# Kernel tuning notes

Measured on AMD Instinct MI355X. Metric: run time of the kernel, lower is better.

## Reference

```python
import jax, jax.numpy as jnp
import numpy as np

H = 16  # n_head

def _rotate_half(x):
    d = x.shape[-1] // 2
    return jnp.concatenate([-x[..., d:], x[..., :d]], axis=-1)

def setup_inputs() -> dict:
    key = jax.random.key(0)
    ks = jax.random.split(key, 12)
    b, t, f, h = 8, 1024, 1024, H
    d = f // h
    inp = {
        "query": jax.random.normal(ks[0], (b, t, f), jnp.float32),
        "key": jax.random.normal(ks[1], (b, t, f), jnp.float32),
        "value": jax.random.normal(ks[2], (b, t, f), jnp.float32),
    }
    # realistic rotary cos/sin, shape (t,1,1,d_k)
    inv_freq = 1.0 / (10000.0 ** (np.arange(0, d, 2, dtype=np.float32) / d))
    pos = np.arange(t, dtype=np.float32)[:, None] * inv_freq[None, :]  # (t, d/2)
    emb = np.concatenate([pos, pos], axis=-1)  # (t, d)
    inp["cos"] = jnp.asarray(np.cos(emb)).reshape(t, 1, 1, d)
    inp["sin"] = jnp.asarray(np.sin(emb)).reshape(t, 1, 1, d)
    inp["mask"] = jax.random.randint(ks[3], (b, t, t), 0, 2) > 0
    s = 1.0 / np.sqrt(f)
    inp["Wq"] = jax.random.normal(ks[4], (f, f), jnp.float32) * s
    inp["bq"] = jax.random.normal(ks[5], (f,), jnp.float32) * 0.02
    inp["Wk"] = jax.random.normal(ks[6], (f, f), jnp.float32) * s
    inp["bk"] = jax.random.normal(ks[7], (f,), jnp.float32) * 0.02
    inp["Wv"] = jax.random.normal(ks[8], (f, f), jnp.float32) * s
    inp["bv"] = jax.random.normal(ks[9], (f,), jnp.float32) * 0.02
    inp["Wo"] = jax.random.normal(ks[10], (f, f), jnp.float32) * s
    inp["bo"] = jax.random.normal(ks[11], (f,), jnp.float32) * 0.02
    return inp

def reference(query, key, value, cos, sin, mask, Wq, bq, Wk, bk, Wv, bv, Wo, bo):
    b, t, f = query.shape
    h = H
    d = f // h
    # RoPE applied pre-projection, per-head layout (b,t,h,d)
    c = cos.reshape(1, t, 1, d)  # broadcast over batch and heads
    s = sin.reshape(1, t, 1, d)
    qr = query.reshape(b, t, h, d)
    kr = key.reshape(b, t, h, d)
    qr = qr * c + _rotate_half(qr) * s
    kr = kr * c + _rotate_half(kr) * s
    q_in = qr.reshape(b, t, f)
    k_in = kr.reshape(b, t, f)
    # QKV projections (nn.Linear: x @ W.T + b), then split heads -> (b,h,t,d)
    q = (jnp.einsum('btf,gf->btg', q_in, Wq) + bq).reshape(b, t, h, d).transpose(0, 2, 1, 3)
    k = (jnp.einsum('btf,gf->btg', k_in, Wk) + bk).reshape(b, t, h, d).transpose(0, 2, 1, 3)
    v = (jnp.einsum('btf,gf->btg', value, Wv) + bv).reshape(b, t, h, d).transpose(0, 2, 1, 3)
    scores = jnp.einsum('bhqd,bhkd->bhqk', q, k) / jnp.sqrt(jnp.asarray(d, q.dtype))
    m = mask[:, None, :, :]  # (b,1,t,t)
    scores = jnp.where(m, jnp.asarray(-10000.0, scores.dtype), scores)
    attn = jax.nn.softmax(scores, axis=-1)
    attn = jnp.where(m, jnp.asarray(0.0, attn.dtype), attn)
    out = jnp.einsum('bhqk,bhkd->bhqd', attn, v)  # (b,h,t,d)
    out = out.transpose(0, 2, 1, 3).reshape(b, t, f)
    return jnp.einsum('btf,gf->btg', out, Wo) + bo
```

## Files before the change

### kernel.cpp

```cpp
#include <hip/hip_runtime.h>
#include <stdint.h>

typedef short short8 __attribute__((ext_vector_type(8)));
typedef float f32x4 __attribute__((ext_vector_type(4)));
typedef unsigned short ushort4v __attribute__((ext_vector_type(4)));
typedef unsigned long long u64;

__device__ __forceinline__ unsigned short f2bf(float f) {
  union { float f; unsigned u; } v; v.f = f;
  unsigned r = v.u + 0x7fffu + ((v.u >> 16) & 1u);
  return (unsigned short)(r >> 16);
}

__device__ __forceinline__ void gld_lds16(const void* g, void* l) {
  __builtin_amdgcn_global_load_lds((const __attribute__((address_space(1))) void*)g,
                                   (__attribute__((address_space(3))) void*)l, 16, 0, 0);
}

__global__ void mask_pack(const int* __restrict__ mask, u64* __restrict__ bits) {
  const int tid = blockIdx.x * 256 + threadIdx.x;
  const int w = tid >> 6, lane = tid & 63;
  const int v = mask[(size_t)w * 64 + lane];
  const u64 b = __ballot(v != 0);
  if (lane == 0) bits[w] = b;
}

__global__ void rope_kernel(const float* __restrict__ q, const float* __restrict__ k,
                            const float* __restrict__ cs, const float* __restrict__ sn,
                            unsigned short* __restrict__ qo, unsigned short* __restrict__ ko) {
  const int idx = blockIdx.x * 256 + threadIdx.x;
  const int p   = idx & 7;
  const int bth = idx >> 3;
  const int t   = (bth >> 4) & 1023;
  const size_t base = (size_t)bth * 64;
  const int dd0 = p * 4;

  const float4 x0 = *(const float4*)(q + base + dd0);
  const float4 x1 = *(const float4*)(q + base + dd0 + 32);
  const float4 y0 = *(const float4*)(k + base + dd0);
  const float4 y1 = *(const float4*)(k + base + dd0 + 32);
  const float4 c0 = *(const float4*)(cs + t * 64 + dd0);
  const float4 c1 = *(const float4*)(cs + t * 64 + dd0 + 32);
  const float4 s0 = *(const float4*)(sn + t * 64 + dd0);
  const float4 s1 = *(const float4*)(sn + t * 64 + dd0 + 32);

  ushort4v qlo, qhi, klo, khi;
  qlo[0]=f2bf(x0.x*c0.x - x1.x*s0.x); qlo[1]=f2bf(x0.y*c0.y - x1.y*s0.y);
  qlo[2]=f2bf(x0.z*c0.z - x1.z*s0.z); qlo[3]=f2bf(x0.w*c0.w - x1.w*s0.w);
  qhi[0]=f2bf(x1.x*c1.x + x0.x*s1.x); qhi[1]=f2bf(x1.y*c1.y + x0.y*s1.y);
  qhi[2]=f2bf(x1.z*c1.z + x0.z*s1.z); qhi[3]=f2bf(x1.w*c1.w + x0.w*s1.w);
  klo[0]=f2bf(y0.x*c0.x - y1.x*s0.x); klo[1]=f2bf(y0.y*c0.y - y1.y*s0.y);
  klo[2]=f2bf(y0.z*c0.z - y1.z*s0.z); klo[3]=f2bf(y0.w*c0.w - y1.w*s0.w);
  khi[0]=f2bf(y1.x*c1.x + y0.x*s1.x); khi[1]=f2bf(y1.y*c1.y + y0.y*s1.y);
  khi[2]=f2bf(y1.z*c1.z + y0.z*s1.z); khi[3]=f2bf(y1.w*c1.w + y0.w*s1.w);

  *(ushort4v*)(qo + base + dd0)      = qlo;
  *(ushort4v*)(qo + base + dd0 + 32) = qhi;
  *(ushort4v*)(ko + base + dd0)      = klo;
  *(ushort4v*)(ko + base + dd0 + 32) = khi;
}

__global__ void cast_kernel(const float* __restrict__ src, unsigned short* __restrict__ dst, int n4) {
  const int i = blockIdx.x * 256 + threadIdx.x;
  if (i < n4) {
    const float4 v = *(const float4*)(src + (size_t)i * 4);
    ushort4v o;
    o[0]=f2bf(v.x); o[1]=f2bf(v.y); o[2]=f2bf(v.z); o[3]=f2bf(v.w);
    *(ushort4v*)(dst + (size_t)i * 4) = o;
  }
}

__global__ void cast4_kernel(const float* __restrict__ s0, const float* __restrict__ s1,
                             const float* __restrict__ s2, const float* __restrict__ s3,
                             unsigned short* __restrict__ d0, unsigned short* __restrict__ d1,
                             unsigned short* __restrict__ d2, unsigned short* __restrict__ d3) {
  const int m = blockIdx.y;
  const float* src = (m == 0) ? s0 : (m == 1) ? s1 : (m == 2) ? s2 : s3;
  unsigned short* dst = (m == 0) ? d0 : (m == 1) ? d1 : (m == 2) ? d2 : d3;
  const int i = blockIdx.x * 256 + threadIdx.x;
  const float4 v = *(const float4*)(src + (size_t)i * 4);
  ushort4v o;
  o[0]=f2bf(v.x); o[1]=f2bf(v.y); o[2]=f2bf(v.z); o[3]=f2bf(v.w);
  *(ushort4v*)(dst + (size_t)i * 4) = o;
}

template <int MODE>
__global__ __launch_bounds__(256, 2) void gemm_bt(
    const unsigned short* __restrict__ A, const unsigned short* __restrict__ Bw,
    const float* __restrict__ bias, void* __restrict__ C) {
  constexpr int K = 1024, N = 1024;
  const int tid = threadIdx.x;
  const int wave = tid >> 6, lane = tid & 63;
  const int m0 = blockIdx.x * 128, n0 = blockIdx.y * 128;
  __shared__ unsigned short Asm[128 * 64];
  __shared__ unsigned short Bsm[128 * 64];
  f32x4 acc[4][4] = {};
  const int wr = (wave >> 1) * 64, wc = (wave & 1) * 64;
  const int ld_row = lane >> 3;
  const int ld_col = ((lane & 7) ^ ld_row) * 8;
  const int fr = lane & 15, g = lane >> 4;
  const int fr7 = fr & 7;

  for (int k0 = 0; k0 < K; k0 += 64) {
#pragma unroll
    for (int j = 0; j < 4; ++j) {
      const int c = j * 4 + wave;
      gld_lds16(A  + (size_t)(m0 + 8 * c + ld_row) * K + k0 + ld_col, &Asm[c * 512]);
      gld_lds16(Bw + (size_t)(n0 + 8 * c + ld_row) * K + k0 + ld_col, &Bsm[c * 512]);
    }
    __syncthreads();
#pragma unroll
    for (int ks = 0; ks < 2; ++ks) {
      const int ch = ((ks * 4 + g) ^ fr7) * 8;
      short8 af[4], bf[4];
#pragma unroll
      for (int i = 0; i < 4; ++i)
        af[i] = *(const short8*)&Asm[(wr + i * 16 + fr) * 64 + ch];
#pragma unroll
      for (int i = 0; i < 4; ++i)
        bf[i] = *(const short8*)&Bsm[(wc + i * 16 + fr) * 64 + ch];
#pragma unroll
      for (int i = 0; i < 4; ++i)
#pragma unroll
        for (int j = 0; j < 4; ++j)
          acc[i][j] = __builtin_amdgcn_mfma_f32_16x16x32_bf16(af[i], bf[j], acc[i][j], 0, 0, 0);
    }
    __syncthreads();
  }

#pragma unroll
  for (int i = 0; i < 4; ++i) {
    const int row_base = m0 + wr + i * 16 + g * 4;
#pragma unroll
    for (int j = 0; j < 4; ++j) {
      const int col = n0 + wc + j * 16 + fr;
      const float bval = bias[col];
      if (MODE == 0) {
        float* Co = (float*)C;
#pragma unroll
        for (int r = 0; r < 4; ++r)
          Co[(size_t)(row_base + r) * N + col] = acc[i][j][r] + bval;
      } else if (MODE == 1) {
        unsigned short* Co = (unsigned short*)C;
        const int h_i = col >> 6, dd = col & 63;
#pragma unroll
        for (int r = 0; r < 4; ++r) {
          const int row = row_base + r;
          const int b_i = row >> 10, t_i = row & 1023;
          Co[((size_t)(b_i * 16 + h_i) * 1024 + t_i) * 64 + dd] = f2bf(acc[i][j][r] + bval);
        }
      } else {
        unsigned short* Co = (unsigned short*)C;
        const int h_i = col >> 6, dd = col & 63;
        const int b_i = row_base >> 10, t_i = row_base & 1023;
        ushort4v pk;
        pk[0] = f2bf(acc[i][j][0] + bval); pk[1] = f2bf(acc[i][j][1] + bval);
        pk[2] = f2bf(acc[i][j][2] + bval); pk[3] = f2bf(acc[i][j][3] + bval);
        *(ushort4v*)&Co[((size_t)(b_i * 16 + h_i) * 64 + dd) * 1024 + t_i] = pk;
      }
    }
  }
}

__global__ __launch_bounds__(256, 2) void flash_attn(
    const unsigned short* __restrict__ Qp, const unsigned short* __restrict__ Kp,
    const unsigned short* __restrict__ Vt, const u64* __restrict__ mbits,
    unsigned short* __restrict__ O) {
  const int bh = blockIdx.x & 127, b_i = bh >> 4, h_i = bh & 15;
  const int q0 = (blockIdx.x >> 7) * 128;
  const int tid = threadIdx.x, wave = tid >> 6, lane = tid & 63;
  const unsigned short* Qb = Qp + (size_t)bh * 65536;
  const unsigned short* Kb = Kp + (size_t)bh * 65536;
  const unsigned short* Vb = Vt + (size_t)bh * 65536;
  const u64* mb = mbits + (size_t)b_i * 16384;

  __shared__ unsigned short smem[16640];
  unsigned short* Vsm = smem;
  unsigned short* Ksm = smem + 8192;
  unsigned short* Pw  = smem + 8192 + wave * 2112;

  const int fr = lane & 15, g = lane >> 4, fr7 = fr & 7;
  const int qw = q0 + wave * 32;

  short8 qf[2][2];
#pragma unroll
  for (int mt = 0; mt < 2; ++mt)
#pragma unroll
    for (int ks = 0; ks < 2; ++ks)
      qf[mt][ks] = *(const short8*)&Qb[(size_t)(qw + mt * 16 + fr) * 64 + ks * 32 + g * 8];

  f32x4 o_acc[2][4] = {};
  float l_run[2][4] = {};

  const int kld_row = lane >> 3;
  const int kld_col = ((lane & 7) ^ kld_row) * 8;
  const int vld_row = lane >> 4;
  const int vld_r7w = 4 * (wave & 1) + vld_row;
  const int vld_col = ((lane & 15) ^ vld_r7w) * 8;

  for (int kt = 0; kt < 1024; kt += 128) {
#pragma unroll
    for (int j = 0; j < 4; ++j) {
      const int c = j * 4 + wave;
      gld_lds16(Kb + (size_t)(kt + 8 * c + kld_row) * 64 + kld_col, &Ksm[c * 512]);
      gld_lds16(Vb + (size_t)(4 * c + vld_row) * 1024 + kt + vld_col, &Vsm[c * 512]);
    }
    __syncthreads();

    f32x4 s_acc[2][8] = {};
#pragma unroll
    for (int ks = 0; ks < 2; ++ks) {
      const int ch = ((ks * 4 + g) ^ fr7) * 8;
      short8 kf[8];
#pragma unroll
      for (int nt = 0; nt < 8; ++nt)
        kf[nt] = *(const short8*)&Ksm[(nt * 16 + fr) * 64 + ch];
#pragma unroll
      for (int mt = 0; mt < 2; ++mt)
#pragma unroll
        for (int nt = 0; nt < 8; ++nt)
          s_acc[mt][nt] = __builtin_amdgcn_mfma_f32_16x16x32_bf16(qf[mt][ks], kf[nt], s_acc[mt][nt], 0, 0, 0);
    }
    __syncthreads();

#pragma unroll
    for (int mt = 0; mt < 2; ++mt) {
#pragma unroll
      for (int r = 0; r < 4; ++r) {
        const int qrow = qw + mt * 16 + g * 4 + r;
        const u64* mrow = &mb[(size_t)qrow * 16 + (kt >> 6)];
        const u64 w0 = mrow[0], w1 = mrow[1];
        float lp = l_run[mt][r];
#pragma unroll
        for (int nt = 0; nt < 8; ++nt) {
          const u64 w = (nt < 4) ? w0 : w1;
          float p = exp2f(s_acc[mt][nt][r] * 0.18033688f);
          p = ((w >> ((nt & 3) * 16 + fr)) & 1) ? 0.0f : p;
          lp += p;
          Pw[(g * 4 + r) * 132 + nt * 16 + fr] = f2bf(p);
        }
        l_run[mt][r] = lp;
      }

#pragma unroll
      for (int ks2 = 0; ks2 < 4; ++ks2) {
        const int vch = ((ks2 * 4 + g) ^ fr7) * 8;
        short8 vf[4];
#pragma unroll
        for (int dt = 0; dt < 4; ++dt)
          vf[dt] = *(const short8*)&Vsm[(dt * 16 + fr) * 128 + vch];
        const short8 pf = *(const short8*)&Pw[fr * 132 + ks2 * 32 + g * 8];
#pragma unroll
        for (int dt = 0; dt < 4; ++dt)
          o_acc[mt][dt] = __builtin_amdgcn_mfma_f32_16x16x32_bf16(pf, vf[dt], o_acc[mt][dt], 0, 0, 0);
      }
    }
    __syncthreads();
  }

#pragma unroll
  for (int mt = 0; mt < 2; ++mt)
#pragma unroll
    for (int r = 0; r < 4; ++r) {
      float l = l_run[mt][r];
#pragma unroll
      for (int off = 1; off < 16; off <<= 1) l += __shfl_xor(l, off, 16);
      const float inv_l = 1.0f / l;
      const int qrow = qw + mt * 16 + g * 4 + r;
#pragma unroll
      for (int dt = 0; dt < 4; ++dt) {
        const int dcol = dt * 16 + fr;
        O[((size_t)(b_i * 1024 + qrow)) * 1024 + h_i * 64 + dcol] = f2bf(o_acc[mt][dt][r] * inv_l);
      }
    }
}

extern "C" void kernel_launch(void* const* d_in, const int* in_sizes, int n_in,
                              void* d_out, int out_size, void* d_ws, size_t ws_size,
                              hipStream_t stream) {
  const float* query = (const float*)d_in[0];
  const float* key   = (const float*)d_in[1];
  const float* value = (const float*)d_in[2];
  const float* cosb  = (const float*)d_in[3];
  const float* sinb  = (const float*)d_in[4];
  const int*   mask  = (const int*)d_in[5];
  const float* Wq = (const float*)d_in[6];
  const float* bq = (const float*)d_in[7];
  const float* Wk = (const float*)d_in[8];
  const float* bk = (const float*)d_in[9];
  const float* Wv = (const float*)d_in[10];
  const float* bv = (const float*)d_in[11];
  const float* Wo = (const float*)d_in[12];
  const float* bo = (const float*)d_in[13];
  (void)in_sizes; (void)n_in; (void)out_size; (void)ws_size;

  char* ws = (char*)d_ws;
  const size_t MB = 1024 * 1024;
  unsigned short* q_in = (unsigned short*)(ws);
  unsigned short* k_in = (unsigned short*)(ws + 16 * MB);
  unsigned short* v_bf = (unsigned short*)(ws + 32 * MB);
  unsigned short* Qp   = (unsigned short*)(ws + 48 * MB);
  unsigned short* Kp   = (unsigned short*)(ws + 64 * MB);
  unsigned short* Vt   = (unsigned short*)(ws + 80 * MB);
  unsigned short* Wqb  = (unsigned short*)(ws + 96 * MB);
  unsigned short* Wkb  = (unsigned short*)(ws + 98 * MB);
  unsigned short* Wvb  = (unsigned short*)(ws + 100 * MB);
  unsigned short* Wob  = (unsigned short*)(ws + 102 * MB);
  u64*            mbits= (u64*)(ws + 104 * MB);
  unsigned short* attn = q_in;

  mask_pack<<<32768, 256, 0, stream>>>(mask, mbits);
  rope_kernel<<<4096, 256, 0, stream>>>(query, key, cosb, sinb, q_in, k_in);
  cast_kernel<<<8192, 256, 0, stream>>>(value, v_bf, 2097152);
  cast4_kernel<<<dim3(1024, 4), 256, 0, stream>>>(Wq, Wk, Wv, Wo, Wqb, Wkb, Wvb, Wob);

  dim3 g(64, 8), blk(256);
  gemm_bt<1><<<g, blk, 0, stream>>>(q_in, Wqb, bq, Qp);
  gemm_bt<1><<<g, blk, 0, stream>>>(k_in, Wkb, bk, Kp);
  gemm_bt<2><<<g, blk, 0, stream>>>(v_bf, Wvb, bv, Vt);
  flash_attn<<<1024, blk, 0, stream>>>(Qp, Kp, Vt, mbits, attn);
  gemm_bt<0><<<g, blk, 0, stream>>>(attn, Wob, bo, d_out);
}
```

Baseline: 409.2 us.

## Permute P/V/mask layouts so attention writes P as packed vectors

Folds the softmax scale into the Q projection epilogue so the attention kernel can call a raw exp2 builtin. The V projection and the mask bit packing now use a permuted key order. This lets each lane own 8 consecutive keys of P, pack them into bf16 pairs with byte permutes, and write one 16-byte vector to a swizzled LDS tile instead of eight scalar stores. The change removes P padding and scalar LDS writes, at the cost of scattered 2-byte global stores in the V epilogue and coupled index permutations that all have to agree.

```diff
diff --git a/kernel.cpp b/kernel.cpp
--- a/kernel.cpp
+++ b/kernel.cpp
@@ -4,7 +4,22 @@
 typedef short short8 __attribute__((ext_vector_type(8)));
 typedef float f32x4 __attribute__((ext_vector_type(4)));
 typedef unsigned short ushort4v __attribute__((ext_vector_type(4)));
+typedef unsigned int uint4v __attribute__((ext_vector_type(4)));
 typedef unsigned long long u64;
+
+#if __has_builtin(__builtin_amdgcn_exp2f)
+#define EXP2(x) __builtin_amdgcn_exp2f(x)
+#else
+#define EXP2(x) exp2f(x)
+#endif
+
+__device__ __forceinline__ unsigned perm_hi16(unsigned hi, unsigned lo) {
+#if __has_builtin(__builtin_amdgcn_perm)
+  return __builtin_amdgcn_perm(hi, lo, 0x07060302u);
+#else
+  return (hi & 0xffff0000u) | (lo >> 16);
+#endif
+}
 
 __device__ __forceinline__ unsigned short f2bf(float f) {
   union { float f; unsigned u; } v; v.f = f;
@@ -20,7 +35,8 @@
 __global__ void mask_pack(const int* __restrict__ mask, u64* __restrict__ bits) {
   const int tid = blockIdx.x * 256 + threadIdx.x;
   const int w = tid >> 6, lane = tid & 63;
-  const int v = mask[(size_t)w * 64 + lane];
+  const int h = w & 1, tb = (w >> 1) & 7, bq = w >> 4;
+  const int v = mask[(size_t)bq * 1024 + tb * 128 + h * 8 + (lane & 7) * 16 + (lane >> 3)];
   const u64 b = __ballot(v != 0);
   if (lane == 0) bits[w] = b;
 }
@@ -87,7 +103,7 @@
 template <int MODE>
 __global__ __launch_bounds__(256, 2) void gemm_bt(
     const unsigned short* __restrict__ A, const unsigned short* __restrict__ Bw,
-    const float* __restrict__ bias, void* __restrict__ C) {
+    const float* __restrict__ bias, void* __restrict__ C, float scale) {
   constexpr int K = 1024, N = 1024;
   const int tid = threadIdx.x;
   const int wave = tid >> 6, lane = tid & 63;
@@ -139,7 +155,7 @@
         float* Co = (float*)C;
 #pragma unroll
         for (int r = 0; r < 4; ++r)
-          Co[(size_t)(row_base + r) * N + col] = acc[i][j][r] + bval;
+          Co[(size_t)(row_base + r) * N + col] = (acc[i][j][r] + bval) * scale;
       } else if (MODE == 1) {
         unsigned short* Co = (unsigned short*)C;
         const int h_i = col >> 6, dd = col & 63;
@@ -147,16 +163,19 @@
         for (int r = 0; r < 4; ++r) {
           const int row = row_base + r;
           const int b_i = row >> 10, t_i = row & 1023;
-          Co[((size_t)(b_i * 16 + h_i) * 1024 + t_i) * 64 + dd] = f2bf(acc[i][j][r] + bval);
+          Co[((size_t)(b_i * 16 + h_i) * 1024 + t_i) * 64 + dd] = f2bf((acc[i][j][r] + bval) * scale);
         }
       } else {
         unsigned short* Co = (unsigned short*)C;
         const int h_i = col >> 6, dd = col & 63;
-        const int b_i = row_base >> 10, t_i = row_base & 1023;
-        ushort4v pk;
-        pk[0] = f2bf(acc[i][j][0] + bval); pk[1] = f2bf(acc[i][j][1] + bval);
-        pk[2] = f2bf(acc[i][j][2] + bval); pk[3] = f2bf(acc[i][j][3] + bval);
-        *(ushort4v*)&Co[((size_t)(b_i * 16 + h_i) * 64 + dd) * 1024 + t_i] = pk;
+#pragma unroll
+        for (int r = 0; r < 4; ++r) {
+          const int row = row_base + r;
+          const int b_i = row >> 10, t_i = row & 1023;
+          const int kp = (t_i & 15) * 8 + ((t_i >> 4) & 7);
+          Co[((size_t)(b_i * 16 + h_i) * 64 + dd) * 1024 + (t_i & ~127) + kp] =
+              f2bf((acc[i][j][r] + bval) * scale);
+        }
       }
     }
   }
@@ -164,20 +183,20 @@
 
 __global__ __launch_bounds__(256, 2) void flash_attn(
     const unsigned short* __restrict__ Qp, const unsigned short* __restrict__ Kp,
-    const unsigned short* __restrict__ Vt, const u64* __restrict__ mbits,
+    const unsigned short* __restrict__ Vp, const u64* __restrict__ mbits,
     unsigned short* __restrict__ O) {
   const int bh = blockIdx.x & 127, b_i = bh >> 4, h_i = bh & 15;
   const int q0 = (blockIdx.x >> 7) * 128;
   const int tid = threadIdx.x, wave = tid >> 6, lane = tid & 63;
   const unsigned short* Qb = Qp + (size_t)bh * 65536;
   const unsigned short* Kb = Kp + (size_t)bh * 65536;
-  const unsigned short* Vb = Vt + (size_t)bh * 65536;
+  const unsigned short* Vb = Vp + (size_t)bh * 65536;
   const u64* mb = mbits + (size_t)b_i * 16384;
 
-  __shared__ unsigned short smem[16640];
+  __shared__ unsigned short smem[16384];
   unsigned short* Vsm = smem;
   unsigned short* Ksm = smem + 8192;
-  unsigned short* Pw  = smem + 8192 + wave * 2112;
+  unsigned short* Pw  = smem + 8192 + wave * 2048;
 
   const int fr = lane & 15, g = lane >> 4, fr7 = fr & 7;
   const int qw = q0 + wave * 32;
@@ -228,28 +247,36 @@
 #pragma unroll
       for (int r = 0; r < 4; ++r) {
         const int qrow = qw + mt * 16 + g * 4 + r;
-        const u64* mrow = &mb[(size_t)qrow * 16 + (kt >> 6)];
-        const u64 w0 = mrow[0], w1 = mrow[1];
+        const u64 w = mb[qrow * 16 + (kt >> 7) * 2 + (fr >> 3)];
+        const unsigned byte8 = (unsigned)(w >> ((fr & 7) * 8)) & 0xffu;
         float lp = l_run[mt][r];
+        unsigned t8[8];
 #pragma unroll
         for (int nt = 0; nt < 8; ++nt) {
-          const u64 w = (nt < 4) ? w0 : w1;
-          float p = exp2f(s_acc[mt][nt][r] * 0.18033688f);
-          p = ((w >> ((nt & 3) * 16 + fr)) & 1) ? 0.0f : p;
-          lp += p;
-          Pw[(g * 4 + r) * 132 + nt * 16 + fr] = f2bf(p);
+          float e = EXP2(s_acc[mt][nt][r]);
+          e = (byte8 & (1u << nt)) ? 0.0f : e;
+          lp += e;
+          union { float f; unsigned u; } cv; cv.f = e;
+          t8[nt] = cv.u + 0x7fffu + ((cv.u >> 16) & 1u);
         }
         l_run[mt][r] = lp;
+        uint4v pk;
+        pk[0] = perm_hi16(t8[1], t8[0]);
+        pk[1] = perm_hi16(t8[3], t8[2]);
+        pk[2] = perm_hi16(t8[5], t8[4]);
+        pk[3] = perm_hi16(t8[7], t8[6]);
+        const int prow = g * 4 + r;
+        *(uint4v*)&Pw[prow * 128 + ((fr ^ (prow & 7)) * 8)] = pk;
       }
 
 #pragma unroll
       for (int ks2 = 0; ks2 < 4; ++ks2) {
-        const int vch = ((ks2 * 4 + g) ^ fr7) * 8;
+        const int cc = (ks2 * 4 + g) ^ fr7;
         short8 vf[4];
 #pragma unroll
         for (int dt = 0; dt < 4; ++dt)
-          vf[dt] = *(const short8*)&Vsm[(dt * 16 + fr) * 128 + vch];
-        const short8 pf = *(const short8*)&Pw[fr * 132 + ks2 * 32 + g * 8];
+          vf[dt] = *(const short8*)&Vsm[(dt * 16 + fr) * 128 + cc * 8];
+        const short8 pf = *(const short8*)&Pw[fr * 128 + cc * 8];
 #pragma unroll
         for (int dt = 0; dt < 4; ++dt)
           o_acc[mt][dt] = __builtin_amdgcn_mfma_f32_16x16x32_bf16(pf, vf[dt], o_acc[mt][dt], 0, 0, 0);
@@ -301,7 +328,7 @@
   unsigned short* v_bf = (unsigned short*)(ws + 32 * MB);
   unsigned short* Qp   = (unsigned short*)(ws + 48 * MB);
   unsigned short* Kp   = (unsigned short*)(ws + 64 * MB);
-  unsigned short* Vt   = (unsigned short*)(ws + 80 * MB);
+  unsigned short* Vp   = (unsigned short*)(ws + 80 * MB);
   unsigned short* Wqb  = (unsigned short*)(ws + 96 * MB);
   unsigned short* Wkb  = (unsigned short*)(ws + 98 * MB);
   unsigned short* Wvb  = (unsigned short*)(ws + 100 * MB);
@@ -315,9 +342,9 @@
   cast4_kernel<<<dim3(1024, 4), 256, 0, stream>>>(Wq, Wk, Wv, Wo, Wqb, Wkb, Wvb, Wob);
 
   dim3 g(64, 8), blk(256);
-  gemm_bt<1><<<g, blk, 0, stream>>>(q_in, Wqb, bq, Qp);
-  gemm_bt<1><<<g, blk, 0, stream>>>(k_in, Wkb, bk, Kp);
-  gemm_bt<2><<<g, blk, 0, stream>>>(v_bf, Wvb, bv, Vt);
-  flash_attn<<<1024, blk, 0, stream>>>(Qp, Kp, Vt, mbits, attn);
-  gemm_bt<0><<<g, blk, 0, stream>>>(attn, Wob, bo, d_out);
-}
+  gemm_bt<1><<<g, blk, 0, stream>>>(q_in, Wqb, bq, Qp, 0.18033688f);
+  gemm_bt<1><<<g, blk, 0, stream>>>(k_in, Wkb, bk, Kp, 1.0f);
+  gemm_bt<2><<<g, blk, 0, stream>>>(v_bf, Wvb, bv, Vp, 1.0f);
+  flash_attn<<<1024, blk, 0, stream>>>(Qp, Kp, Vp, mbits, attn);
+  gemm_bt<0><<<g, blk, 0, stream>>>(attn, Wob, bo, d_out, 1.0f);
+}
```

After: 375.4 us. 1.09x faster.
